# Performance work log

Hardware: AMD Instinct MI355X
Metric: run time of the kernel (lower is better)

The kernel has to match this reference:

```python
import jax, jax.numpy as jnp
import numpy as np

B, S, E, H = 2, 2048, 1024, 8
DH = E // H


def setup_inputs() -> dict:
    key = jax.random.key(0)
    ks = jax.random.split(key, 8)
    sc = 1.0 / np.sqrt(E)
    return {
        "q": jax.random.normal(ks[0], (B, S, E), jnp.float32),
        "k": jax.random.normal(ks[1], (B, S, E), jnp.float32),
        "v": jax.random.normal(ks[2], (B, S, E), jnp.float32),
        "Wq": jax.random.normal(ks[3], (E, E), jnp.float32) * sc,
        "bq": jnp.zeros((E,), jnp.float32),
        "Wk": jax.random.normal(ks[4], (E, E), jnp.float32) * sc,
        "bk": jnp.zeros((E,), jnp.float32),
        "Wv": jax.random.normal(ks[5], (E, E), jnp.float32) * sc,
        "bv": jnp.zeros((E,), jnp.float32),
        "Wo": jax.random.normal(ks[6], (E, E), jnp.float32) * sc,
        "bo": jnp.zeros((E,), jnp.float32),
        "is_causal": 1,
    }


def reference(q, k, v, Wq, bq, Wk, bk, Wv, bv, Wo, bo, is_causal):
    # q,k,v: [B,S,E]. Dense projections, split into H heads of dim DH.
    def heads(x, W, b):
        y = x @ W + b                       # [B,S,E]
        return y.reshape(B, S, H, DH).transpose(0, 2, 1, 3)  # [B,H,S,DH]

    qh = heads(q, Wq, bq)
    kh = heads(k, Wk, bk)
    vh = heads(v, Wv, bv)

    scale = 1.0 / jnp.sqrt(jnp.asarray(DH, q.dtype))
    scores = jnp.einsum("bhsd,bhtd->bhst", qh, kh) * scale  # [B,H,S,S]

    if is_causal:
        # tril mask (BigBird layout is all-ones here; causality comes from attn_mask)
        causal = jnp.tril(jnp.ones((S, S), bool))
        neg = jnp.asarray(jnp.finfo(scores.dtype).min, scores.dtype)
        scores = jnp.where(causal[None, None], scores, neg)

    attn = jax.nn.softmax(scores, axis=-1)                  # [B,H,S,S]
    ctx = jnp.einsum("bhst,bhtd->bhsd", attn, vh)           # [B,H,S,DH]
    ctx = ctx.transpose(0, 2, 1, 3).reshape(B, S, E)        # merge heads
    return ctx @ Wo + bo
```

## Files before the change

### kernel.cpp

```cpp
#include <hip/hip_runtime.h>
#include <math.h>


typedef __bf16 bf16_t;
typedef __bf16 bf16x8 __attribute__((ext_vector_type(8)));
typedef float f32x4 __attribute__((ext_vector_type(4)));

#define MFMA16(a, b, c) __builtin_amdgcn_mfma_f32_16x16x32_bf16(a, b, c, 0, 0, 0)

__global__ __launch_bounds__(256) void prep(const float* q, const float* k,
                                            const float* v, bf16_t* qb,
                                            bf16_t* kb, bf16_t* vb,
                                            const float* W0, const float* W1,
                                            const float* W2, const float* W3,
                                            bf16_t* Wt) {
  const int bid = blockIdx.x, tid = threadIdx.x;
  if (bid < 6144) {
    const int z = bid >> 11, chunk = bid & 2047;
    const float* x = (z == 0) ? q : (z == 1) ? k : v;
    bf16_t* y = (z == 0) ? qb : (z == 1) ? kb : vb;
    size_t i = ((size_t)chunk * 256 + tid) * 8;
    float4 a = *(const float4*)(x + i);
    float4 b = *(const float4*)(x + i + 4);
    bf16x8 o = {(bf16_t)a.x, (bf16_t)a.y, (bf16_t)a.z, (bf16_t)a.w,
                (bf16_t)b.x, (bf16_t)b.y, (bf16_t)b.z, (bf16_t)b.w};
    *(bf16x8*)(y + i) = o;
  } else {
    __shared__ float t[32][33];
    const int b2 = bid - 6144;
    const int wz = b2 >> 10, t2 = b2 & 1023;
    const float* W = (wz == 0) ? W0 : (wz == 1) ? W1 : (wz == 2) ? W2 : W3;
    bf16_t* o = Wt + (size_t)wz * 1024 * 1024;
    const int n0 = (t2 & 31) * 32, k0 = (t2 >> 5) * 32;
    const int tx = tid & 31, ty = tid >> 5;
#pragma unroll
    for (int i = 0; i < 4; i++)
      t[ty + 8 * i][tx] = W[(size_t)(k0 + ty + 8 * i) * 1024 + n0 + tx];
    __syncthreads();
#pragma unroll
    for (int i = 0; i < 4; i++)
      o[(size_t)(n0 + ty + 8 * i) * 1024 + k0 + tx] = (bf16_t)t[tx][ty + 8 * i];
  }
}

template <int MODE>
__global__ __launch_bounds__(256) void gemm_k(
    const bf16_t* qb, const bf16_t* kb, const bf16_t* vb, const bf16_t* Wt,
    const float* b0, const float* b1, const float* b2, bf16_t* Qh, bf16_t* Kh,
    bf16_t* Vt, float* Of32) {
  __shared__ bf16_t As[2][128 * 64];
  __shared__ bf16_t Bs[2][128 * 64];
  const int tid = threadIdx.x, w = tid >> 6, lane = tid & 63;
  const int bm = blockIdx.y, bn = blockIdx.x;
  const int wr = w >> 1, wc = w & 1, q4 = lane >> 4, lo = lane & 15;
  const int z = (MODE == 0) ? blockIdx.z : 3;
  const bf16_t* A = (MODE == 1) ? qb : (z == 0) ? qb : (z == 1) ? kb : vb;
  const bf16_t* Bt = Wt + (size_t)z * 1024 * 1024;
  const float* bias = (MODE == 1) ? b0 : (z == 0) ? b0 : (z == 1) ? b1 : b2;

  f32x4 acc[4][4];
#pragma unroll
  for (int m = 0; m < 4; m++)
#pragma unroll
    for (int n = 0; n < 4; n++) acc[m][n] = (f32x4){0.f, 0.f, 0.f, 0.f};

  const int r2 = tid >> 1;
  const int cb = (tid & 1) * 4;
  const bf16_t* Arow = A + (size_t)(bm * 128 + r2) * 1024;
  const bf16_t* Brow = Bt + (size_t)(bn * 128 + r2) * 1024;

  bf16x8 ar[4], br[4];
  auto loadAB = [&](int k0) {
#pragma unroll
    for (int i = 0; i < 4; i++) {
      ar[i] = *(const bf16x8*)(Arow + k0 + (cb + i) * 8);
      br[i] = *(const bf16x8*)(Brow + k0 + (cb + i) * 8);
    }
  };

  loadAB(0);
  for (int k = 0; k < 16; k++) {
    const int cur = k & 1;
#pragma unroll
    for (int i = 0; i < 4; i++) {
      *(bf16x8*)&As[cur][r2 * 64 + (((cb + i) ^ (r2 & 7)) * 8)] = ar[i];
      *(bf16x8*)&Bs[cur][r2 * 64 + (((cb + i) ^ (r2 & 7)) * 8)] = br[i];
    }
    if (k < 15) loadAB((k + 1) * 64);
    __syncthreads();

#pragma unroll
    for (int kc = 0; kc < 2; kc++) {
      bf16x8 af[4], bfr[4];
#pragma unroll
      for (int m = 0; m < 4; m++) {
        int rr = wr * 64 + m * 16 + lo;
        af[m] = *(const bf16x8*)&As[cur][rr * 64 + (((kc * 4 + q4) ^ (rr & 7)) * 8)];
      }
#pragma unroll
      for (int n = 0; n < 4; n++) {
        int rr = wc * 64 + n * 16 + lo;
        bfr[n] = *(const bf16x8*)&Bs[cur][rr * 64 + (((kc * 4 + q4) ^ (rr & 7)) * 8)];
      }
#pragma unroll
      for (int m = 0; m < 4; m++)
#pragma unroll
        for (int n = 0; n < 4; n++)
          acc[m][n] = MFMA16(af[m], bfr[n], acc[m][n]);
    }
  }

#pragma unroll
  for (int m = 0; m < 4; m++) {
#pragma unroll
    for (int n = 0; n < 4; n++) {
      int rowg0 = bm * 128 + wr * 64 + m * 16 + q4 * 4;
      int colg = bn * 128 + wc * 64 + n * 16 + lo;
      float bv = bias[colg];
#pragma unroll
      for (int rg = 0; rg < 4; rg++) {
        float val = acc[m][n][rg] + bv;
        int row = rowg0 + rg;
        if (MODE == 1) {
          Of32[(size_t)row * 1024 + colg] = val;
        } else {
          int b = row >> 11, s = row & 2047;
          int h = colg >> 7, d = colg & 127;
          if (z == 0)
            Qh[(((size_t)(b * 8 + h)) * 2048 + s) * 128 + d] = (bf16_t)val;
          else if (z == 1)
            Kh[(((size_t)(b * 8 + h)) * 2048 + s) * 128 + d] = (bf16_t)val;
          else
            Vt[(((size_t)(b * 8 + h)) * 128 + d) * 2048 + s] = (bf16_t)val;
        }
      }
    }
  }
}

__global__ __launch_bounds__(256) void flash_k(const bf16_t* Qh,
                                               const bf16_t* Kh,
                                               const bf16_t* Vt, bf16_t* ctx,
                                               const int* causal_p) {
  __shared__ bf16_t sm[32768 + 4 * 1280];
  const int tid = threadIdx.x, w = tid >> 6, lane = tid & 63;
  const int q4 = lane >> 4, lo = lane & 15;
  const int n0 = blockIdx.x;
  const int u = n0 & 255, hi = n0 >> 8;
  const int bh = u & 15, p0 = u >> 4;
  const int t = hi ? (31 - p0) : p0;
  const int causal = *causal_p;
  const int kmax = causal ? t : 31;

  bf16_t* Ps = sm + 32768 + w * 1280;

  bf16x8 aq[4];
  {
    const bf16_t* qa = Qh + ((size_t)bh * 2048 + t * 64 + w * 16 + lo) * 128;
#pragma unroll
    for (int ks = 0; ks < 4; ks++) aq[ks] = *(const bf16x8*)(qa + ks * 32 + q4 * 8);
  }

  const bf16_t* Kbase = Kh + (size_t)bh * 2048 * 128;
  const bf16_t* Vbase = Vt + (size_t)bh * 128 * 2048;
  const int kr = tid >> 2, kc = (tid & 3) * 4;
  const int vd = tid >> 1, vc = (tid & 1) * 4;

  bf16x8 kreg[4], vreg[4];
  auto loadKV = [&](int kt) {
    const bf16_t* kp = Kbase + (size_t)(kt * 64 + kr) * 128;
    const bf16_t* vp = Vbase + (size_t)vd * 2048 + kt * 64;
#pragma unroll
    for (int i = 0; i < 4; i++) {
      kreg[i] = *(const bf16x8*)(kp + (kc + i) * 8);
      vreg[i] = *(const bf16x8*)(vp + (vc + i) * 8);
    }
  };

  f32x4 acc[8], lacc;
#pragma unroll
  for (int i = 0; i < 8; i++) acc[i] = (f32x4){0.f, 0.f, 0.f, 0.f};
  lacc = (f32x4){0.f, 0.f, 0.f, 0.f};

  const bf16_t one = (bf16_t)1.0f;
  const bf16x8 vone = {one, one, one, one, one, one, one, one};
  const float sc2 = 0.08838834764831845f * 1.44269504088896f;

  loadKV(0);
  for (int kt = 0; kt <= kmax; ++kt) {
    bf16_t* Kd = sm + (kt & 1) * 8192;
    bf16_t* Vd = sm + 16384 + (kt & 1) * 8192;
#pragma unroll
    for (int i = 0; i < 4; i++)
      *(bf16x8*)&Kd[kr * 128 + (((kc + i) ^ (kr & 7)) * 8)] = kreg[i];
#pragma unroll
    for (int i = 0; i < 4; i++)
      *(bf16x8*)&Vd[vd * 64 + (((vc + i) ^ ((vd >> 1) & 7)) * 8)] = vreg[i];
    if (kt < kmax) loadKV(kt + 1);
    __syncthreads();

    f32x4 sa[4];
#pragma unroll
    for (int nt = 0; nt < 4; nt++) sa[nt] = (f32x4){0.f, 0.f, 0.f, 0.f};
#pragma unroll
    for (int ks = 0; ks < 4; ks++) {
#pragma unroll
      for (int nt = 0; nt < 4; nt++) {
        int key = nt * 16 + lo;
        bf16x8 bk =
            *(const bf16x8*)&Kd[key * 128 + (((ks * 4 + q4) ^ (key & 7)) * 8)];
        sa[nt] = MFMA16(aq[ks], bk, sa[nt]);
      }
    }

    const bool diag = causal && (kt == t);
    const int rloc = w * 16 + q4 * 4;
#pragma unroll
    for (int nt = 0; nt < 4; nt++) {
      int key = nt * 16 + lo;
#pragma unroll
      for (int rg = 0; rg < 4; rg++) {
        float pv = exp2f(sa[nt][rg] * sc2);
        if (diag && key > rloc + rg) pv = 0.f;
        Ps[(q4 * 4 + rg) * 80 + key] = (bf16_t)pv;
      }
    }

    bf16x8 ap0 = *(const bf16x8*)&Ps[lo * 80 + q4 * 8];
    bf16x8 ap1 = *(const bf16x8*)&Ps[lo * 80 + 32 + q4 * 8];
    lacc = MFMA16(ap0, vone, lacc);
    lacc = MFMA16(ap1, vone, lacc);
#pragma unroll
    for (int n = 0; n < 8; n++) {
      int d = n * 16 + lo;
      int sw = (d >> 1) & 7;
      bf16x8 bv0 = *(const bf16x8*)&Vd[d * 64 + ((q4 ^ sw) * 8)];
      bf16x8 bv1 = *(const bf16x8*)&Vd[d * 64 + (((4 + q4) ^ sw) * 8)];
      acc[n] = MFMA16(ap0, bv0, acc[n]);
      acc[n] = MFMA16(ap1, bv1, acc[n]);
    }
  }

  int b = bh >> 3, h = bh & 7;
#pragma unroll
  for (int rg = 0; rg < 4; rg++) {
    float inv = 1.f / lacc[rg];
    int r = b * 2048 + t * 64 + w * 16 + q4 * 4 + rg;
#pragma unroll
    for (int n = 0; n < 8; n++)
      ctx[(size_t)r * 1024 + h * 128 + n * 16 + lo] = (bf16_t)(acc[n][rg] * inv);
  }
}

extern "C" void kernel_launch(void* const* d_in, const int* in_sizes, int n_in,
                              void* d_out, int out_size, void* d_ws,
                              size_t ws_size, hipStream_t stream) {
  const float* q = (const float*)d_in[0];
  const float* k = (const float*)d_in[1];
  const float* v = (const float*)d_in[2];
  const float* Wq = (const float*)d_in[3];
  const float* bq = (const float*)d_in[4];
  const float* Wk = (const float*)d_in[5];
  const float* bk = (const float*)d_in[6];
  const float* Wv = (const float*)d_in[7];
  const float* bv = (const float*)d_in[8];
  const float* Wo = (const float*)d_in[9];
  const float* bo = (const float*)d_in[10];
  const int* isc = (const int*)d_in[11];

  char* ws = (char*)d_ws;
  bf16_t* Wt = (bf16_t*)ws;
  bf16_t* qb = (bf16_t*)(ws + (8ull << 20));
  bf16_t* kb = (bf16_t*)(ws + (16ull << 20));
  bf16_t* vb = (bf16_t*)(ws + (24ull << 20));
  bf16_t* Qh = (bf16_t*)(ws + (32ull << 20));
  bf16_t* Kh = (bf16_t*)(ws + (40ull << 20));
  bf16_t* Vt = (bf16_t*)(ws + (48ull << 20));
  bf16_t* ctx = (bf16_t*)(ws + (8ull << 20));

  prep<<<dim3(10240), 256, 0, stream>>>(q, k, v, qb, kb, vb, Wq, Wk, Wv, Wo, Wt);

  gemm_k<0><<<dim3(8, 32, 3), 256, 0, stream>>>(qb, kb, vb, Wt, bq, bk, bv, Qh,
                                                Kh, Vt, nullptr);

  flash_k<<<dim3(512), 256, 0, stream>>>(Qh, Kh, Vt, ctx, isc);

  gemm_k<1><<<dim3(8, 32), 256, 0, stream>>>(ctx, nullptr, nullptr, Wt, bo,
                                             nullptr, nullptr, nullptr, nullptr,
                                             nullptr, (float*)d_out);
}
```

Before: 231.7 us.

## Load K/V MFMA fragments directly from global memory, dropping LDS staging

The flash attention kernel stops staging K and V tiles through double-buffered shared memory and instead has each lane load its MFMA B-operand fragments straight from global memory (relying on L1/L2 to catch reuse across the four waves). This removes the LDS stores and the per-iteration __syncthreads, shrinks shared memory to the per-wave P buffer, whose row stride changes from 80 to 88, and adds a min-blocks launch bound of 4 for higher occupancy. The cost is that each wave now fetches the full K/V tile separately, so global/cache traffic rises by roughly 4x and the loads are no longer prefetched one tile ahead. Load latency is exposed unless occupancy hides it.

```diff
diff --git a/kernel.cpp b/kernel.cpp
--- a/kernel.cpp
+++ b/kernel.cpp
@@ -138,11 +138,11 @@
   }
 }
 
-__global__ __launch_bounds__(256) void flash_k(const bf16_t* Qh,
-                                               const bf16_t* Kh,
-                                               const bf16_t* Vt, bf16_t* ctx,
-                                               const int* causal_p) {
-  __shared__ bf16_t sm[32768 + 4 * 1280];
+__global__ __launch_bounds__(256, 4) void flash_k(const bf16_t* Qh,
+                                                  const bf16_t* Kh,
+                                                  const bf16_t* Vt, bf16_t* ctx,
+                                                  const int* causal_p) {
+  __shared__ bf16_t Pbuf[4 * 16 * 88];
   const int tid = threadIdx.x, w = tid >> 6, lane = tid & 63;
   const int q4 = lane >> 4, lo = lane & 15;
   const int n0 = blockIdx.x;
@@ -152,7 +152,7 @@
   const int causal = *causal_p;
   const int kmax = causal ? t : 31;
 
-  bf16_t* Ps = sm + 32768 + w * 1280;
+  bf16_t* Ps = Pbuf + w * (16 * 88);
 
   bf16x8 aq[4];
   {
@@ -161,21 +161,8 @@
     for (int ks = 0; ks < 4; ks++) aq[ks] = *(const bf16x8*)(qa + ks * 32 + q4 * 8);
   }
 
-  const bf16_t* Kbase = Kh + (size_t)bh * 2048 * 128;
-  const bf16_t* Vbase = Vt + (size_t)bh * 128 * 2048;
-  const int kr = tid >> 2, kc = (tid & 3) * 4;
-  const int vd = tid >> 1, vc = (tid & 1) * 4;
-
-  bf16x8 kreg[4], vreg[4];
-  auto loadKV = [&](int kt) {
-    const bf16_t* kp = Kbase + (size_t)(kt * 64 + kr) * 128;
-    const bf16_t* vp = Vbase + (size_t)vd * 2048 + kt * 64;
-#pragma unroll
-    for (int i = 0; i < 4; i++) {
-      kreg[i] = *(const bf16x8*)(kp + (kc + i) * 8);
-      vreg[i] = *(const bf16x8*)(vp + (vc + i) * 8);
-    }
-  };
+  const bf16_t* Kb = Kh + ((size_t)bh * 2048 + lo) * 128 + q4 * 8;
+  const bf16_t* Vb = Vt + ((size_t)bh * 128 + lo) * 2048 + q4 * 8;
 
   f32x4 acc[8], lacc;
 #pragma unroll
@@ -186,19 +173,8 @@
   const bf16x8 vone = {one, one, one, one, one, one, one, one};
   const float sc2 = 0.08838834764831845f * 1.44269504088896f;
 
-  loadKV(0);
   for (int kt = 0; kt <= kmax; ++kt) {
-    bf16_t* Kd = sm + (kt & 1) * 8192;
-    bf16_t* Vd = sm + 16384 + (kt & 1) * 8192;
-#pragma unroll
-    for (int i = 0; i < 4; i++)
-      *(bf16x8*)&Kd[kr * 128 + (((kc + i) ^ (kr & 7)) * 8)] = kreg[i];
-#pragma unroll
-    for (int i = 0; i < 4; i++)
-      *(bf16x8*)&Vd[vd * 64 + (((vc + i) ^ ((vd >> 1) & 7)) * 8)] = vreg[i];
-    if (kt < kmax) loadKV(kt + 1);
-    __syncthreads();
-
+    const bf16_t* Kt = Kb + (size_t)kt * 64 * 128;
     f32x4 sa[4];
 #pragma unroll
     for (int nt = 0; nt < 4; nt++) sa[nt] = (f32x4){0.f, 0.f, 0.f, 0.f};
@@ -206,9 +182,7 @@
     for (int ks = 0; ks < 4; ks++) {
 #pragma unroll
       for (int nt = 0; nt < 4; nt++) {
-        int key = nt * 16 + lo;
-        bf16x8 bk =
-            *(const bf16x8*)&Kd[key * 128 + (((ks * 4 + q4) ^ (key & 7)) * 8)];
+        bf16x8 bk = *(const bf16x8*)(Kt + nt * (16 * 128) + ks * 32);
         sa[nt] = MFMA16(aq[ks], bk, sa[nt]);
       }
     }
@@ -222,20 +196,20 @@
       for (int rg = 0; rg < 4; rg++) {
         float pv = exp2f(sa[nt][rg] * sc2);
         if (diag && key > rloc + rg) pv = 0.f;
-        Ps[(q4 * 4 + rg) * 80 + key] = (bf16_t)pv;
-      }
-    }
-
-    bf16x8 ap0 = *(const bf16x8*)&Ps[lo * 80 + q4 * 8];
-    bf16x8 ap1 = *(const bf16x8*)&Ps[lo * 80 + 32 + q4 * 8];
+        Ps[(q4 * 4 + rg) * 88 + key] = (bf16_t)pv;
+      }
+    }
+
+    bf16x8 ap0 = *(const bf16x8*)&Ps[lo * 88 + q4 * 8];
+    bf16x8 ap1 = *(const bf16x8*)&Ps[lo * 88 + 32 + q4 * 8];
     lacc = MFMA16(ap0, vone, lacc);
     lacc = MFMA16(ap1, vone, lacc);
+
+    const bf16_t* Vtt = Vb + kt * 64;
 #pragma unroll
     for (int n = 0; n < 8; n++) {
-      int d = n * 16 + lo;
-      int sw = (d >> 1) & 7;
-      bf16x8 bv0 = *(const bf16x8*)&Vd[d * 64 + ((q4 ^ sw) * 8)];
-      bf16x8 bv1 = *(const bf16x8*)&Vd[d * 64 + (((4 + q4) ^ sw) * 8)];
+      bf16x8 bv0 = *(const bf16x8*)(Vtt + (size_t)n * (16 * 2048));
+      bf16x8 bv1 = *(const bf16x8*)(Vtt + (size_t)n * (16 * 2048) + 32);
       acc[n] = MFMA16(ap0, bv0, acc[n]);
       acc[n] = MFMA16(ap1, bv1, acc[n]);
     }
```

Result: slower. 377.8 us (+63.0%).

## Use direct global-to-LDS loads in projection GEMM and repad P scratch

Applied to the files above, without the earlier changes.

The projection GEMM now stages its A and B tiles with global_load_lds, which writes straight into shared memory. This replaces the old path of loading into registers and then storing to LDS. The XOR swizzle moves into the global-address side, and the prefetch for the next buffer is issued right after the barrier. Separately, the flash kernel's per-warp P scratch row stride changes from 80 to 88 elements to reduce LDS bank conflicts, at the cost of slightly more shared memory.

```diff
diff --git a/kernel.cpp b/kernel.cpp
--- a/kernel.cpp
+++ b/kernel.cpp
@@ -7,6 +7,11 @@
 typedef float f32x4 __attribute__((ext_vector_type(4)));
 
 #define MFMA16(a, b, c) __builtin_amdgcn_mfma_f32_16x16x32_bf16(a, b, c, 0, 0, 0)
+
+#define GLD16(gp, lp)                                                     \
+  __builtin_amdgcn_global_load_lds(                                       \
+      (const __attribute__((address_space(1))) void*)(gp),                \
+      (__attribute__((address_space(3))) void*)(lp), 16, 0, 0)
 
 __global__ __launch_bounds__(256) void prep(const float* q, const float* k,
                                             const float* v, bf16_t* qb,
@@ -64,30 +69,25 @@
 #pragma unroll
     for (int n = 0; n < 4; n++) acc[m][n] = (f32x4){0.f, 0.f, 0.f, 0.f};
 
-  const int r2 = tid >> 1;
-  const int cb = (tid & 1) * 4;
-  const bf16_t* Arow = A + (size_t)(bm * 128 + r2) * 1024;
-  const bf16_t* Brow = Bt + (size_t)(bn * 128 + r2) * 1024;
-
-  bf16x8 ar[4], br[4];
-  auto loadAB = [&](int k0) {
-#pragma unroll
-    for (int i = 0; i < 4; i++) {
-      ar[i] = *(const bf16x8*)(Arow + k0 + (cb + i) * 8);
-      br[i] = *(const bf16x8*)(Brow + k0 + (cb + i) * 8);
+  const int srow = w * 32 + (lane >> 3);
+  const int schunk = (lane & 7) ^ (lane >> 3);
+  const bf16_t* gA = A + (size_t)(bm * 128 + srow) * 1024 + schunk * 8;
+  const bf16_t* gB = Bt + (size_t)(bn * 128 + srow) * 1024 + schunk * 8;
+  const int ldsrow = w * 32;
+
+  auto stage = [&](int buf, int k0) {
+#pragma unroll
+    for (int j = 0; j < 4; j++) {
+      GLD16(gA + k0 + j * 8192, &As[buf][(ldsrow + j * 8) * 64]);
+      GLD16(gB + k0 + j * 8192, &Bs[buf][(ldsrow + j * 8) * 64]);
     }
   };
 
-  loadAB(0);
+  stage(0, 0);
   for (int k = 0; k < 16; k++) {
     const int cur = k & 1;
-#pragma unroll
-    for (int i = 0; i < 4; i++) {
-      *(bf16x8*)&As[cur][r2 * 64 + (((cb + i) ^ (r2 & 7)) * 8)] = ar[i];
-      *(bf16x8*)&Bs[cur][r2 * 64 + (((cb + i) ^ (r2 & 7)) * 8)] = br[i];
-    }
-    if (k < 15) loadAB((k + 1) * 64);
     __syncthreads();
+    if (k < 15) stage(cur ^ 1, (k + 1) * 64);
 
 #pragma unroll
     for (int kc = 0; kc < 2; kc++) {
@@ -142,7 +142,7 @@
                                                const bf16_t* Kh,
                                                const bf16_t* Vt, bf16_t* ctx,
                                                const int* causal_p) {
-  __shared__ bf16_t sm[32768 + 4 * 1280];
+  __shared__ bf16_t sm[32768 + 4 * 1408];
   const int tid = threadIdx.x, w = tid >> 6, lane = tid & 63;
   const int q4 = lane >> 4, lo = lane & 15;
   const int n0 = blockIdx.x;
@@ -152,7 +152,7 @@
   const int causal = *causal_p;
   const int kmax = causal ? t : 31;
 
-  bf16_t* Ps = sm + 32768 + w * 1280;
+  bf16_t* Ps = sm + 32768 + w * 1408;
 
   bf16x8 aq[4];
   {
@@ -222,12 +222,12 @@
       for (int rg = 0; rg < 4; rg++) {
         float pv = exp2f(sa[nt][rg] * sc2);
         if (diag && key > rloc + rg) pv = 0.f;
-        Ps[(q4 * 4 + rg) * 80 + key] = (bf16_t)pv;
-      }
-    }
-
-    bf16x8 ap0 = *(const bf16x8*)&Ps[lo * 80 + q4 * 8];
-    bf16x8 ap1 = *(const bf16x8*)&Ps[lo * 80 + 32 + q4 * 8];
+        Ps[(q4 * 4 + rg) * 88 + key] = (bf16_t)pv;
+      }
+    }
+
+    bf16x8 ap0 = *(const bf16x8*)&Ps[lo * 88 + q4 * 8];
+    bf16x8 ap1 = *(const bf16x8*)&Ps[lo * 88 + 32 + q4 * 8];
     lacc = MFMA16(ap0, vone, lacc);
     lacc = MFMA16(ap1, vone, lacc);
 #pragma unroll
```

Measured after the change: 246.0 us. 6.1% more time.
